# Kernel tuning notes

Hardware: AMD Instinct MI355X
Metric: run time of the kernel (lower is better)

Reference implementation:

```python
import jax, jax.numpy as jnp
import numpy as np

DMODEL = 1024
DK = 64
DHEAD = 16
DEPTH = DK * DHEAD
N, LQ, L = 2, 2048, 2048


def setup_inputs() -> dict:
    key = jax.random.key(0)
    ks = jax.random.split(key, 12)
    s = 1.0 / np.sqrt(DMODEL)
    inp = {
        'x': jax.random.normal(ks[0], (N, LQ, DMODEL), jnp.float32),
        'y': jax.random.normal(ks[1], (N, L, DMODEL), jnp.float32),
        'mask': jnp.tril(jnp.ones((LQ, L), dtype=bool)),  # causal
        'Wq': jax.random.normal(ks[2], (DMODEL, DEPTH), jnp.float32) * s,
        'bq': jnp.zeros((DEPTH,), jnp.float32),
        'Wk': jax.random.normal(ks[3], (DMODEL, DEPTH), jnp.float32) * s,
        'bk': jnp.zeros((DEPTH,), jnp.float32),
        'Wv': jax.random.normal(ks[4], (DMODEL, DEPTH), jnp.float32) * s,
        'bv': jnp.zeros((DEPTH,), jnp.float32),
        'Wo': jax.random.normal(ks[5], (DEPTH, DMODEL), jnp.float32) * (1.0 / np.sqrt(DEPTH)),
        'bo': jnp.zeros((DMODEL,), jnp.float32),
    }
    return inp


def reference(x, y, mask, Wq, bq, Wk, bk, Wv, bv, Wo, bo):
    fac = 1.0 / np.sqrt(DK)
    q = (x @ Wq + bq).reshape(N, LQ, DHEAD, DK).transpose(0, 2, 1, 3)  # N,H,Lq,dk
    k = (y @ Wk + bk).reshape(N, L, DHEAD, DK).transpose(0, 2, 1, 3)   # N,H,L,dk
    v = (y @ Wv + bv).reshape(N, L, DHEAD, DK).transpose(0, 2, 1, 3)   # N,H,L,dk
    scores = jnp.einsum('bhqd,bhkd->bhqk', q, k) * fac                 # N,H,Lq,L
    scores = jnp.where(mask, scores, -1e9)  # mask broadcasts over N,H
    attn = jax.nn.softmax(scores, axis=-1)
    out = jnp.einsum('bhqk,bhkd->bhqd', attn, v)                        # N,H,Lq,dk
    out = out.transpose(0, 2, 1, 3).reshape(N, LQ, DEPTH)
    return out @ Wo + bo
```

## Files before the change

kernel.cpp:

```cpp
#include <hip/hip_runtime.h>
#include <hip/hip_bf16.h>

typedef __attribute__((ext_vector_type(8))) short short8;
typedef __attribute__((ext_vector_type(4))) float floatx4;

#define LQ 2048
#define DM 1024
#define NH 16
#define LOG2E 1.44269504088896f

typedef __attribute__((address_space(1))) void gas_t;
typedef __attribute__((address_space(3))) void las_t;

__device__ __forceinline__ void async16(const __hip_bfloat16* g, __hip_bfloat16* l) {
    __builtin_amdgcn_global_load_lds((gas_t*)g, (las_t*)l, 16, 0, 0);
}

__global__ __launch_bounds__(256) void prep_all(
    const float* __restrict__ x,  const float* __restrict__ y,
    const float* __restrict__ Wq, const float* __restrict__ Wk,
    const float* __restrict__ Wv, const float* __restrict__ Wo,
    __hip_bfloat16* __restrict__ xb,  __hip_bfloat16* __restrict__ yb,
    __hip_bfloat16* __restrict__ Wqt, __hip_bfloat16* __restrict__ Wkt,
    __hip_bfloat16* __restrict__ Wvt, __hip_bfloat16* __restrict__ Wot)
{
    __shared__ float tile[64][65];
    const int t  = threadIdx.x;
    const int bx = blockIdx.x;

    if (bx < 4096) {
        const float* in = (bx < 2048) ? x : y;
        __hip_bfloat16* out = (bx < 2048) ? xb : yb;
        const int i = ((bx & 2047) * 256 + t) * 8;
        float4 a0 = ((const float4*)(in + i))[0];
        float4 a1 = ((const float4*)(in + i))[1];
        union { __hip_bfloat16 h[8]; uint4 u; } pk;
        pk.h[0] = __float2bfloat16(a0.x); pk.h[1] = __float2bfloat16(a0.y);
        pk.h[2] = __float2bfloat16(a0.z); pk.h[3] = __float2bfloat16(a0.w);
        pk.h[4] = __float2bfloat16(a1.x); pk.h[5] = __float2bfloat16(a1.y);
        pk.h[6] = __float2bfloat16(a1.z); pk.h[7] = __float2bfloat16(a1.w);
        *(uint4*)(out + i) = pk.u;
        return;
    }

    const int r    = bx - 4096;
    const int wsel = r >> 8;
    const int tid  = r & 255;
    const int n0   = (tid & 15) * 64, k0 = (tid >> 4) * 64;
    const float* W = (wsel == 0) ? Wq : (wsel == 1) ? Wk : (wsel == 2) ? Wv : Wo;
    __hip_bfloat16* Wt = (wsel == 0) ? Wqt : (wsel == 1) ? Wkt : (wsel == 2) ? Wvt : Wot;

    const int rr0 = t >> 4, c4 = (t & 15) * 4;
#pragma unroll
    for (int rr = 0; rr < 64; rr += 16) {
        float4 v = *(const float4*)&W[(size_t)(k0 + rr0 + rr) * DM + n0 + c4];
        tile[rr0 + rr][c4 + 0] = v.x; tile[rr0 + rr][c4 + 1] = v.y;
        tile[rr0 + rr][c4 + 2] = v.z; tile[rr0 + rr][c4 + 3] = v.w;
    }
    __syncthreads();
    const int nr = t >> 2, kc = (t & 3) * 16;
    union { __hip_bfloat16 h[16]; uint4 u[2]; } pk;
#pragma unroll
    for (int i = 0; i < 16; ++i) pk.h[i] = __float2bfloat16(tile[kc + i][nr]);
    uint4* dst = (uint4*)&Wt[(size_t)(n0 + nr) * DM + k0 + kc];
    dst[0] = pk.u[0];
    dst[1] = pk.u[1];
}

__global__ __launch_bounds__(512, 4) void gemm_qkv(
    const __hip_bfloat16* __restrict__ xb,
    const __hip_bfloat16* __restrict__ yb,
    const __hip_bfloat16* __restrict__ Bt,
    const float* __restrict__ bq, const float* __restrict__ bk,
    const float* __restrict__ bv,
    __hip_bfloat16* __restrict__ Qb, __hip_bfloat16* __restrict__ Kb,
    __hip_bfloat16* __restrict__ Vt,
    float qscl)
{
    constexpr int BM = 256, BN = 128, Kd = 1024;
    constexpr int NHS = Kd / 32;
    __shared__ __align__(16) __hip_bfloat16 As[3][BM * 32];
    __shared__ __align__(16) __hip_bfloat16 Bs[3][BN * 32];

    const int t    = threadIdx.x;
    const int w    = t >> 6;
    const int lane = t & 63;
    const int quad = lane >> 4;
    const int l16  = lane & 15;
    const int wm   = w & 3;
    const int wn   = w >> 2;

    const int f  = blockIdx.x;
    const int rx = f & 7;
    const int rr = f >> 3;
    const int bx = (rx & 3) * 6 + rr % 6;
    const int by = (rx >> 2) * 8 + rr / 6;
    const int m0 = by * BM;
    const int n0 = bx * BN;

    const int region = n0 >> 10;
    const int nl     = n0 & 1023;

    const __hip_bfloat16* A = (region == 0) ? xb : yb;

    floatx4 acc[4][4];
#pragma unroll
    for (int i = 0; i < 4; ++i)
#pragma unroll
        for (int j = 0; j < 4; ++j) acc[i][j] = (floatx4){0.f, 0.f, 0.f, 0.f};

    auto stageA = [&](int h) {
        const int k0 = h * 32, slot = h % 3;
#pragma unroll
        for (int l = 0; l < 2; ++l) {
            const int c   = l * 512 + t;
            const int row = c >> 2;
            const int ch  = (c & 3) ^ ((row >> 1) & 3);
            async16(A + (size_t)(m0 + row) * Kd + k0 + ch * 8, &As[slot][c * 8]);
        }
    };
    auto stageB = [&](int h) {
        const int k0 = h * 32, slot = h % 3;
        const int c   = t;
        const int row = c >> 2;
        const int ch  = (c & 3) ^ ((row >> 1) & 3);
        async16(Bt + (size_t)(n0 + row) * Kd + k0 + ch * 8, &Bs[slot][c * 8]);
    };

    stageA(0); stageB(0); stageA(1); stageB(1);
    asm volatile("s_waitcnt vmcnt(3)" ::: "memory");
    __builtin_amdgcn_sched_barrier(0);
    __builtin_amdgcn_s_barrier();

    const int csw = (l16 >> 1) & 3;

    for (int h = 0; h < NHS; ++h) {
        const int slot = h % 3;
        const __hip_bfloat16* as = &As[slot][0];
        const __hip_bfloat16* bs = &Bs[slot][0];
        short8 af[4], bf[4];

#pragma unroll
        for (int nj = 0; nj < 4; ++nj) {
            const int row = wn * 64 + nj * 16 + l16;
            bf[nj] = *(const short8*)&bs[row * 32 + (quad ^ csw) * 8];
        }
#pragma unroll
        for (int mi = 0; mi < 2; ++mi) {
            const int row = wm * 64 + mi * 16 + l16;
            af[mi] = *(const short8*)&as[row * 32 + (quad ^ csw) * 8];
        }
        if (h + 2 < NHS) stageA(h + 2);
        __builtin_amdgcn_s_barrier();
        asm volatile("s_waitcnt lgkmcnt(0)" ::: "memory");
        __builtin_amdgcn_sched_barrier(0);
        __builtin_amdgcn_s_setprio(1);
#pragma unroll
        for (int mi = 0; mi < 2; ++mi)
#pragma unroll
            for (int nj = 0; nj < 4; ++nj)
                acc[mi][nj] = __builtin_amdgcn_mfma_f32_16x16x32_bf16(af[mi], bf[nj], acc[mi][nj], 0, 0, 0);
        __builtin_amdgcn_s_setprio(0);
        __builtin_amdgcn_s_barrier();

#pragma unroll
        for (int mi = 2; mi < 4; ++mi) {
            const int row = wm * 64 + mi * 16 + l16;
            af[mi] = *(const short8*)&as[row * 32 + (quad ^ csw) * 8];
        }
        if (h + 2 < NHS) stageB(h + 2);
        __builtin_amdgcn_s_barrier();
        asm volatile("s_waitcnt lgkmcnt(0)" ::: "memory");
        __builtin_amdgcn_sched_barrier(0);
        __builtin_amdgcn_s_setprio(1);
#pragma unroll
        for (int mi = 2; mi < 4; ++mi)
#pragma unroll
            for (int nj = 0; nj < 4; ++nj)
                acc[mi][nj] = __builtin_amdgcn_mfma_f32_16x16x32_bf16(af[mi], bf[nj], acc[mi][nj], 0, 0, 0);
        __builtin_amdgcn_s_setprio(0);
        if (h + 2 < NHS)      asm volatile("s_waitcnt vmcnt(3)" ::: "memory");
        else                  asm volatile("s_waitcnt vmcnt(0)" ::: "memory");
        __builtin_amdgcn_sched_barrier(0);
        __builtin_amdgcn_s_barrier();
    }

    if (region < 2) {
        __hip_bfloat16* C    = (region == 0) ? Qb : Kb;
        const float*    bias = (region == 0) ? bq : bk;
        const float     scl  = (region == 0) ? qscl : 1.0f;
#pragma unroll
        for (int j = 0; j < 4; ++j) {
            const int col = nl + wn * 64 + j * 16 + l16;
            const float bvv = bias[col];
#pragma unroll
            for (int mi = 0; mi < 4; ++mi) {
#pragma unroll
                for (int r = 0; r < 4; ++r) {
                    const int row = m0 + wm * 64 + mi * 16 + quad * 4 + r;
                    C[(size_t)row * 1024 + col] = __float2bfloat16((acc[mi][j][r] + bvv) * scl);
                }
            }
        }
    } else {
#pragma unroll
        for (int j = 0; j < 4; ++j) {
            const int col = nl + wn * 64 + j * 16 + l16;
            const float bvv = bv[col];
#pragma unroll
            for (int mi = 0; mi < 4; ++mi) {
                const int row0 = m0 + wm * 64 + mi * 16 + quad * 4;
                union { __hip_bfloat16 h4[4]; uint2 u; } pk;
#pragma unroll
                for (int r = 0; r < 4; ++r)
                    pk.h4[r] = __float2bfloat16(acc[mi][j][r] + bvv);
                *(uint2*)&Vt[((size_t)((row0 >> 11) * 1024 + col)) * 2048 + (row0 & 2047)] = pk.u;
            }
        }
    }
}

__global__ __launch_bounds__(256) void gemm_o(
    const __hip_bfloat16* __restrict__ A,
    const __hip_bfloat16* __restrict__ Bt,
    const float* __restrict__ bias,
    float* __restrict__ C,
    int M)
{
    constexpr int BM = 64, BN = 128, BK = 32, Kd = 1024, NIT = Kd / BK;
    __shared__ __align__(16) __hip_bfloat16 As[3][BM * BK];
    __shared__ __align__(16) __hip_bfloat16 Bs[3][BN * BK];

    const int t    = threadIdx.x;
    const int w    = t >> 6;
    const int lane = t & 63;
    const int quad = lane >> 4;
    const int l16  = lane & 15;
    const int wm   = w & 1;
    const int wn   = w >> 1;

    const int f  = blockIdx.x;
    const int rx = f & 7;
    const int rr = f >> 3;
    const int bx = (rx & 1) * 4 + (rr & 3);
    const int by = (rx >> 1) * 16 + (rr >> 2);
    const int m0 = by * BM;
    const int n0 = bx * BN;

    const int lrow = lane >> 2;
    const int lcol = (lane & 3) * 8;

    floatx4 acc[2][4];
#pragma unroll
    for (int i = 0; i < 2; ++i)
#pragma unroll
        for (int j = 0; j < 4; ++j) acc[i][j] = (floatx4){0.f, 0.f, 0.f, 0.f};

    auto stage = [&](int k0, int buf) {
#pragma unroll
        for (int s = 0; s < 3; ++s) {
            const int seg = w * 3 + s;
            if (seg < 4) {
                async16(A + (size_t)(m0 + seg * 16 + lrow) * Kd + k0 + lcol,
                        &As[buf][seg * 16 * BK]);
            } else {
                const int bs = seg - 4;
                async16(Bt + (size_t)(n0 + bs * 16 + lrow) * Kd + k0 + lcol,
                        &Bs[buf][bs * 16 * BK]);
            }
        }
    };

    stage(0, 0);
    stage(BK, 1);
    int cur = 0;
    for (int i = 0; i < NIT; ++i) {
        if (i < NIT - 1) asm volatile("s_waitcnt vmcnt(3)" ::: "memory");
        else             asm volatile("s_waitcnt vmcnt(0)" ::: "memory");
        __builtin_amdgcn_sched_barrier(0);
        __builtin_amdgcn_s_barrier();
        if (i + 2 < NIT) stage((i + 2) * BK, (cur + 2 >= 3) ? cur - 1 : cur + 2);

        short8 af[2], bf[4];
#pragma unroll
        for (int ii = 0; ii < 2; ++ii)
            af[ii] = *(const short8*)&As[cur][(wm * 32 + ii * 16 + l16) * BK + quad * 8];
#pragma unroll
        for (int j = 0; j < 4; ++j)
            bf[j] = *(const short8*)&Bs[cur][(wn * 64 + j * 16 + l16) * BK + quad * 8];
#pragma unroll
        for (int ii = 0; ii < 2; ++ii)
#pragma unroll
            for (int j = 0; j < 4; ++j)
                acc[ii][j] = __builtin_amdgcn_mfma_f32_16x16x32_bf16(af[ii], bf[j], acc[ii][j], 0, 0, 0);
        cur = (cur + 1 >= 3) ? 0 : cur + 1;
    }

#pragma unroll
    for (int j = 0; j < 4; ++j) {
        const int col = n0 + wn * 64 + j * 16 + l16;
        const float bvf = bias[col];
#pragma unroll
        for (int i = 0; i < 2; ++i) {
#pragma unroll
            for (int r = 0; r < 4; ++r) {
                const int row = m0 + wm * 32 + i * 16 + quad * 4 + r;
                C[(size_t)row * 1024 + col] = acc[i][j][r] + bvf;
            }
        }
    }
}

template <bool A_IS_F32, bool OUT_F32, bool TRANSV = false>
__global__ __launch_bounds__(256) void gemm64(
    const void* __restrict__ Av,
    const float* __restrict__ B,
    const float* __restrict__ bias,
    void* __restrict__ Cv,
    int M, int N, int K, float scale)
{
    __shared__ __align__(16) __hip_bfloat16 As[64][40];
    __shared__ __align__(16) __hip_bfloat16 Bs[64][40];

    const int t    = threadIdx.x;
    const int wave = t >> 6;
    const int lane = t & 63;
    const int quad = lane >> 4;
    const int l16  = lane & 15;
    const int m0   = blockIdx.y * 64;
    const int n0   = blockIdx.x * 64;

    floatx4 acc[4];
#pragma unroll
    for (int i = 0; i < 4; ++i) acc[i] = (floatx4){0.f, 0.f, 0.f, 0.f};

    const int arow = t >> 2, acol = (t & 3) * 8;
    const int bkk  = t >> 3, bnn  = (t & 7) * 8;

    for (int k0 = 0; k0 < K; k0 += 32) {
        if constexpr (A_IS_F32) {
            const float* A = (const float*)Av;
            const float* ap = A + (size_t)(m0 + arow) * K + k0 + acol;
            float4 a0 = ((const float4*)ap)[0];
            float4 a1 = ((const float4*)ap)[1];
            union { __hip_bfloat16 h[8]; short8 s; } up;
            up.h[0] = __float2bfloat16(a0.x); up.h[1] = __float2bfloat16(a0.y);
            up.h[2] = __float2bfloat16(a0.z); up.h[3] = __float2bfloat16(a0.w);
            up.h[4] = __float2bfloat16(a1.x); up.h[5] = __float2bfloat16(a1.y);
            up.h[6] = __float2bfloat16(a1.z); up.h[7] = __float2bfloat16(a1.w);
            *(short8*)(&As[arow][acol]) = up.s;
        } else {
            const __hip_bfloat16* A = (const __hip_bfloat16*)Av;
            uint4 av = *(const uint4*)(A + (size_t)(m0 + arow) * K + k0 + acol);
            *(uint4*)(&As[arow][acol]) = av;
        }
        {
            const float* bp = B + (size_t)(k0 + bkk) * N + n0 + bnn;
            float4 b0 = ((const float4*)bp)[0];
            float4 b1 = ((const float4*)bp)[1];
            Bs[bnn + 0][bkk] = __float2bfloat16(b0.x);
            Bs[bnn + 1][bkk] = __float2bfloat16(b0.y);
            Bs[bnn + 2][bkk] = __float2bfloat16(b0.z);
            Bs[bnn + 3][bkk] = __float2bfloat16(b0.w);
            Bs[bnn + 4][bkk] = __float2bfloat16(b1.x);
            Bs[bnn + 5][bkk] = __float2bfloat16(b1.y);
            Bs[bnn + 6][bkk] = __float2bfloat16(b1.z);
            Bs[bnn + 7][bkk] = __float2bfloat16(b1.w);
        }
        __syncthreads();

        short8 afrag = *(const short8*)(&As[wave * 16 + l16][quad * 8]);
#pragma unroll
        for (int nt = 0; nt < 4; ++nt) {
            short8 bfrag = *(const short8*)(&Bs[nt * 16 + l16][quad * 8]);
            acc[nt] = __builtin_amdgcn_mfma_f32_16x16x32_bf16(afrag, bfrag, acc[nt], 0, 0, 0);
        }
        __syncthreads();
    }

#pragma unroll
    for (int nt = 0; nt < 4; ++nt) {
        const int col = n0 + nt * 16 + l16;
        const float bvf = bias[col];
        if constexpr (TRANSV) {
            const int row0 = m0 + wave * 16 + quad * 4;
            union { __hip_bfloat16 h4[4]; uint2 u; } pk;
#pragma unroll
            for (int r = 0; r < 4; ++r)
                pk.h4[r] = __float2bfloat16(acc[nt][r] + bvf);
            *(uint2*)&((__hip_bfloat16*)Cv)[((size_t)((row0 >> 11) * 1024 + col)) * 2048 + (row0 & 2047)] = pk.u;
        } else {
#pragma unroll
            for (int r = 0; r < 4; ++r) {
                const int row = m0 + wave * 16 + quad * 4 + r;
                const float v = (acc[nt][r] + bvf) * scale;
                if constexpr (OUT_F32) ((float*)Cv)[(size_t)row * N + col] = v;
                else ((__hip_bfloat16*)Cv)[(size_t)row * N + col] = __float2bfloat16(v);
            }
        }
    }
}

#define PP 72

__global__ __launch_bounds__(256, 2) void attn_mfma11(
    const __hip_bfloat16* __restrict__ Q,
    const __hip_bfloat16* __restrict__ K,
    const __hip_bfloat16* __restrict__ Vt,
    __hip_bfloat16* __restrict__ O)
{
    __shared__ __align__(16) __hip_bfloat16 KtS[3][64 * 64];
    __shared__ __align__(16) __hip_bfloat16 VtS[4][64 * 64];
    __shared__ __align__(16) __hip_bfloat16 PsQ[128 * PP];

    const int t    = threadIdx.x;
    const int w    = t >> 6;
    const int lane = t & 63;
    const int quad = lane >> 4;
    const int l16  = lane & 15;

    const int f   = blockIdx.x;
    const int xcd = f & 7;
    const int u   = f >> 3;
    const int pi  = u >> 4;
    const int qr  = u & 15;
    const int qx  = (pi & 2) ? (15 - qr) : qr;
    const int p   = xcd * 4 + pi;
    const int h   = p & 15;
    const int b   = p >> 4;
    const int q0  = qx * 128;

    const size_t rowbase = (size_t)b * LQ;
    const int    hcol    = h * 64;
    const size_t vbase   = (size_t)(b * NH + h) * 64 * LQ;

    const int r8 = l16 & 7;

    auto stage = [&](int j0n, int jtile) {
        const int ks = jtile % 3;
        const int vs = jtile & 3;
#pragma unroll
        for (int rnd = 0; rnd < 2; ++rnd) {
            const int c   = rnd * 256 + t;
            const int row = c >> 3;
            const int ch  = (c & 7) ^ (row & 7);
            async16(K + (rowbase + j0n + row) * DM + hcol + ch * 8,
                    &KtS[ks][c * 8]);
            async16(Vt + vbase + (size_t)row * LQ + j0n + ch * 8,
                    &VtS[vs][c * 8]);
        }
    };

    {
        const int qrow = t >> 1, qseg = (t & 1) * 32;
        const uint4* src = (const uint4*)(Q + (rowbase + q0 + qrow) * DM + hcol + qseg);
        uint4* dst = (uint4*)&PsQ[qrow * PP + qseg];
        dst[0] = src[0]; dst[1] = src[1]; dst[2] = src[2]; dst[3] = src[3];
    }
    stage(0, 0);
    stage(64, 1);

    short8 qf[2][2];
#pragma unroll
    for (int g = 0; g < 2; ++g)
#pragma unroll
        for (int hh = 0; hh < 2; ++hh)
            qf[g][hh] = *(const short8*)&PsQ[(w * 32 + g * 16 + l16) * PP + hh * 32 + quad * 8];

    __hip_bfloat16* Pw = &PsQ[(w * 32) * PP];

    float l_i[2] = {0.f, 0.f};
    floatx4 o[2][4];
#pragma unroll
    for (int g = 0; g < 2; ++g)
#pragma unroll
        for (int i = 0; i < 4; ++i) o[g][i] = (floatx4){0.f, 0.f, 0.f, 0.f};

    const int wq_lo  = q0 + w * 32;
    const int wq_hi  = wq_lo + 31;
    const int ntiles = 2 * qx + 2;

    short8 pa[2][2];
    int    pslot = -1;

    for (int jt = 0; jt < ntiles; ++jt) {
        const int j0 = jt * 64;

        if (jt < ntiles - 1) asm volatile("s_waitcnt vmcnt(4)" ::: "memory");
        else                 asm volatile("s_waitcnt vmcnt(0)" ::: "memory");
        __builtin_amdgcn_sched_barrier(0);
        __builtin_amdgcn_s_barrier();
        if (jt + 2 < ntiles) stage(j0 + 128, jt + 2);

        const bool active = (j0 <= wq_hi);

        short8 ak[4][2];
        if (active) {
#pragma unroll
            for (int jc = 0; jc < 4; ++jc) {
                const __hip_bfloat16* kr = &KtS[jt % 3][(jc * 16 + l16) * 64];
                ak[jc][0] = *(const short8*)&kr[((quad    ) ^ r8) * 8];
                ak[jc][1] = *(const short8*)&kr[((quad + 4) ^ r8) * 8];
            }
        }

        if (pslot >= 0) {
            __builtin_amdgcn_s_setprio(1);
#pragma unroll
            for (int subf = 0; subf < 4; ++subf) {
                const __hip_bfloat16* vr = &VtS[pslot][(subf * 16 + l16) * 64];
                short8 vb0 = *(const short8*)&vr[((quad    ) ^ r8) * 8];
                short8 vb1 = *(const short8*)&vr[((quad + 4) ^ r8) * 8];
#pragma unroll
                for (int g = 0; g < 2; ++g) {
                    o[g][subf] = __builtin_amdgcn_mfma_f32_16x16x32_bf16(pa[g][0], vb0, o[g][subf], 0, 0, 0);
                    o[g][subf] = __builtin_amdgcn_mfma_f32_16x16x32_bf16(pa[g][1], vb1, o[g][subf], 0, 0, 0);
                }
            }
            __builtin_amdgcn_s_setprio(0);
            pslot = -1;
        }

        if (active) {
            const bool bnd = (j0 + 63 > wq_lo);
            __builtin_amdgcn_s_setprio(1);
#pragma unroll
            for (int jc = 0; jc < 4; ++jc) {
#pragma unroll
                for (int g = 0; g < 2; ++g) {
                    floatx4 z = (floatx4){0.f, 0.f, 0.f, 0.f};
                    z = __builtin_amdgcn_mfma_f32_16x16x32_bf16(ak[jc][0], qf[g][0], z, 0, 0, 0);
                    z = __builtin_amdgcn_mfma_f32_16x16x32_bf16(ak[jc][1], qf[g][1], z, 0, 0, 0);
                    if (bnd) {
                        const int qg = wq_lo + g * 16 + l16;
#pragma unroll
                        for (int r = 0; r < 4; ++r) {
                            const int j = j0 + jc * 16 + quad * 4 + r;
                            if (j > qg) z[r] = -1e30f;
                        }
                    }
                    union { __hip_bfloat16 h4[4]; uint2 u; } pk;
#pragma unroll
                    for (int r = 0; r < 4; ++r) {
                        const float e = __builtin_amdgcn_exp2f(z[r]);
                        l_i[g] += e;
                        pk.h4[r] = __float2bfloat16(e);
                    }
                    *(uint2*)&Pw[(g * 16 + l16) * PP + jc * 16 + quad * 4] = pk.u;
                }
            }
            __builtin_amdgcn_s_setprio(0);
#pragma unroll
            for (int g = 0; g < 2; ++g) {
                pa[g][0] = *(const short8*)&Pw[(g * 16 + l16) * PP + quad * 8];
                pa[g][1] = *(const short8*)&Pw[(g * 16 + l16) * PP + 32 + quad * 8];
            }
            pslot = jt & 3;
        }
    }

    if (pslot >= 0) {
#pragma unroll
        for (int subf = 0; subf < 4; ++subf) {
            const __hip_bfloat16* vr = &VtS[pslot][(subf * 16 + l16) * 64];
            short8 vb0 = *(const short8*)&vr[((quad    ) ^ r8) * 8];
            short8 vb1 = *(const short8*)&vr[((quad + 4) ^ r8) * 8];
#pragma unroll
            for (int g = 0; g < 2; ++g) {
                o[g][subf] = __builtin_amdgcn_mfma_f32_16x16x32_bf16(pa[g][0], vb0, o[g][subf], 0, 0, 0);
                o[g][subf] = __builtin_amdgcn_mfma_f32_16x16x32_bf16(pa[g][1], vb1, o[g][subf], 0, 0, 0);
            }
        }
    }

#pragma unroll
    for (int g = 0; g < 2; ++g) {
        l_i[g] += __shfl_xor(l_i[g], 16);
        l_i[g] += __shfl_xor(l_i[g], 32);
#pragma unroll
        for (int r = 0; r < 4; ++r) {
            const float linv = 1.0f / __shfl(l_i[g], quad * 4 + r);
            const size_t row = rowbase + q0 + w * 32 + g * 16 + quad * 4 + r;
#pragma unroll
            for (int subf = 0; subf < 4; ++subf)
                O[row * DM + hcol + subf * 16 + l16] = __float2bfloat16(o[g][subf][r] * linv);
        }
    }
}

extern "C" void kernel_launch(void* const* d_in, const int* in_sizes, int n_in,
                              void* d_out, int out_size, void* d_ws, size_t ws_size,
                              hipStream_t stream)
{
    (void)in_sizes; (void)n_in; (void)out_size;

    const float* x  = (const float*)d_in[0];
    const float* y  = (const float*)d_in[1];
    const float* Wq = (const float*)d_in[3];
    const float* bq = (const float*)d_in[4];
    const float* Wk = (const float*)d_in[5];
    const float* bk = (const float*)d_in[6];
    const float* Wv = (const float*)d_in[7];
    const float* bv = (const float*)d_in[8];
    const float* Wo = (const float*)d_in[9];
    const float* bo = (const float*)d_in[10];

    const size_t NTOK = (size_t)2 * LQ * DM;
    const size_t MM   = (size_t)DM * DM;
    const int    M    = 2 * LQ;
    const float  QSCL = 0.125f * LOG2E;

    __hip_bfloat16* Qb  = (__hip_bfloat16*)d_ws;
    __hip_bfloat16* Kb  = Qb + NTOK;
    __hip_bfloat16* Vtb = Kb + NTOK;
    __hip_bfloat16* Ab  = Vtb + NTOK;

    const size_t need = (4 * NTOK + 2 * NTOK + 4 * MM) * sizeof(__hip_bfloat16);
    const dim3 agrid(512, 1, 1);

    if (ws_size >= need) {
        __hip_bfloat16* xb  = Ab + NTOK;
        __hip_bfloat16* yb  = xb + NTOK;
        __hip_bfloat16* Wqt = yb + NTOK;
        __hip_bfloat16* Wkt = Wqt + MM;
        __hip_bfloat16* Wvt = Wkt + MM;
        __hip_bfloat16* Wot = Wvt + MM;
        (void)Wkt; (void)Wvt;

        prep_all<<<5120, 256, 0, stream>>>(x, y, Wq, Wk, Wv, Wo,
                                           xb, yb, Wqt, Wkt, Wvt, Wot);

        gemm_qkv<<<384, 512, 0, stream>>>(xb, yb, Wqt, bq, bk, bv, Qb, Kb, Vtb, QSCL);
        attn_mfma11<<<agrid, 256, 0, stream>>>(Qb, Kb, Vtb, Ab);
        gemm_o<<<512, 256, 0, stream>>>(Ab, Wot, bo, (float*)d_out, M);
    } else {
        const dim3 gblk(DM / 64, M / 64);
        gemm64<true,  false><<<gblk, 256, 0, stream>>>(x, Wq, bq, Qb, M, DM, DM, QSCL);
        gemm64<true,  false><<<gblk, 256, 0, stream>>>(y, Wk, bk, Kb, M, DM, DM, 1.0f);
        gemm64<true,  false, true><<<gblk, 256, 0, stream>>>(y, Wv, bv, Vtb, M, DM, DM, 1.0f);
        attn_mfma11<<<agrid, 256, 0, stream>>>(Qb, Kb, Vtb, Ab);
        gemm64<false, true ><<<gblk, 256, 0, stream>>>(Ab, Wo, bo, (float*)d_out, M, DM, DM, 1.0f);
    }
}
```

Baseline: 208.9 us.

## Split attention block across 8 waves of 16 query rows each

The attention kernel now runs 512 threads per block, with each wave owning 16 query rows instead of 32. Staging loads are spread over twice as many threads, and per-wave registers for Q fragments, accumulators and P are halved. The aim is more waves in flight to hide latency and finer causal skipping per wave. In exchange, each wave gets less MFMA reuse of K/V fragments read from LDS, doubling LDS reads per FLOP, and it raises barrier participation cost.

```diff
diff --git a/kernel.cpp b/kernel.cpp
--- a/kernel.cpp
+++ b/kernel.cpp
@@ -403,7 +403,7 @@
 
 #define PP 72
 
-__global__ __launch_bounds__(256, 2) void attn_mfma11(
+__global__ __launch_bounds__(512, 4) void attn_mfma12(
     const __hip_bfloat16* __restrict__ Q,
     const __hip_bfloat16* __restrict__ K,
     const __hip_bfloat16* __restrict__ Vt,
@@ -439,54 +439,47 @@
     auto stage = [&](int j0n, int jtile) {
         const int ks = jtile % 3;
         const int vs = jtile & 3;
-#pragma unroll
-        for (int rnd = 0; rnd < 2; ++rnd) {
-            const int c   = rnd * 256 + t;
-            const int row = c >> 3;
-            const int ch  = (c & 7) ^ (row & 7);
-            async16(K + (rowbase + j0n + row) * DM + hcol + ch * 8,
-                    &KtS[ks][c * 8]);
-            async16(Vt + vbase + (size_t)row * LQ + j0n + ch * 8,
-                    &VtS[vs][c * 8]);
-        }
+        const int c   = t;
+        const int row = c >> 3;
+        const int ch  = (c & 7) ^ (row & 7);
+        async16(K + (rowbase + j0n + row) * DM + hcol + ch * 8,
+                &KtS[ks][c * 8]);
+        async16(Vt + vbase + (size_t)row * LQ + j0n + ch * 8,
+                &VtS[vs][c * 8]);
     };
 
     {
-        const int qrow = t >> 1, qseg = (t & 1) * 32;
+        const int qrow = t >> 2, qseg = (t & 3) * 16;
         const uint4* src = (const uint4*)(Q + (rowbase + q0 + qrow) * DM + hcol + qseg);
         uint4* dst = (uint4*)&PsQ[qrow * PP + qseg];
-        dst[0] = src[0]; dst[1] = src[1]; dst[2] = src[2]; dst[3] = src[3];
+        dst[0] = src[0]; dst[1] = src[1];
     }
     stage(0, 0);
     stage(64, 1);
 
-    short8 qf[2][2];
-#pragma unroll
-    for (int g = 0; g < 2; ++g)
-#pragma unroll
-        for (int hh = 0; hh < 2; ++hh)
-            qf[g][hh] = *(const short8*)&PsQ[(w * 32 + g * 16 + l16) * PP + hh * 32 + quad * 8];
-
-    __hip_bfloat16* Pw = &PsQ[(w * 32) * PP];
-
-    float l_i[2] = {0.f, 0.f};
-    floatx4 o[2][4];
-#pragma unroll
-    for (int g = 0; g < 2; ++g)
-#pragma unroll
-        for (int i = 0; i < 4; ++i) o[g][i] = (floatx4){0.f, 0.f, 0.f, 0.f};
-
-    const int wq_lo  = q0 + w * 32;
-    const int wq_hi  = wq_lo + 31;
+    short8 qf[2];
+#pragma unroll
+    for (int hh = 0; hh < 2; ++hh)
+        qf[hh] = *(const short8*)&PsQ[(w * 16 + l16) * PP + hh * 32 + quad * 8];
+
+    __hip_bfloat16* Pw = &PsQ[(w * 16) * PP];
+
+    float l_i = 0.f;
+    floatx4 o[4];
+#pragma unroll
+    for (int i = 0; i < 4; ++i) o[i] = (floatx4){0.f, 0.f, 0.f, 0.f};
+
+    const int wq_lo  = q0 + w * 16;
+    const int wq_hi  = wq_lo + 15;
     const int ntiles = 2 * qx + 2;
 
-    short8 pa[2][2];
+    short8 pa[2];
     int    pslot = -1;
 
     for (int jt = 0; jt < ntiles; ++jt) {
         const int j0 = jt * 64;
 
-        if (jt < ntiles - 1) asm volatile("s_waitcnt vmcnt(4)" ::: "memory");
+        if (jt < ntiles - 1) asm volatile("s_waitcnt vmcnt(2)" ::: "memory");
         else                 asm volatile("s_waitcnt vmcnt(0)" ::: "memory");
         __builtin_amdgcn_sched_barrier(0);
         __builtin_amdgcn_s_barrier();
@@ -511,11 +504,8 @@
                 const __hip_bfloat16* vr = &VtS[pslot][(subf * 16 + l16) * 64];
                 short8 vb0 = *(const short8*)&vr[((quad    ) ^ r8) * 8];
                 short8 vb1 = *(const short8*)&vr[((quad + 4) ^ r8) * 8];
-#pragma unroll
-                for (int g = 0; g < 2; ++g) {
-                    o[g][subf] = __builtin_amdgcn_mfma_f32_16x16x32_bf16(pa[g][0], vb0, o[g][subf], 0, 0, 0);
-                    o[g][subf] = __builtin_amdgcn_mfma_f32_16x16x32_bf16(pa[g][1], vb1, o[g][subf], 0, 0, 0);
-                }
+                o[subf] = __builtin_amdgcn_mfma_f32_16x16x32_bf16(pa[0], vb0, o[subf], 0, 0, 0);
+                o[subf] = __builtin_amdgcn_mfma_f32_16x16x32_bf16(pa[1], vb1, o[subf], 0, 0, 0);
             }
             __builtin_amdgcn_s_setprio(0);
             pslot = -1;
@@ -526,35 +516,29 @@
             __builtin_amdgcn_s_setprio(1);
 #pragma unroll
             for (int jc = 0; jc < 4; ++jc) {
-#pragma unroll
-                for (int g = 0; g < 2; ++g) {
-                    floatx4 z = (floatx4){0.f, 0.f, 0.f, 0.f};
-                    z = __builtin_amdgcn_mfma_f32_16x16x32_bf16(ak[jc][0], qf[g][0], z, 0, 0, 0);
-                    z = __builtin_amdgcn_mfma_f32_16x16x32_bf16(ak[jc][1], qf[g][1], z, 0, 0, 0);
-                    if (bnd) {
-                        const int qg = wq_lo + g * 16 + l16;
-#pragma unroll
-                        for (int r = 0; r < 4; ++r) {
-                            const int j = j0 + jc * 16 + quad * 4 + r;
-                            if (j > qg) z[r] = -1e30f;
-                        }
+                floatx4 z = (floatx4){0.f, 0.f, 0.f, 0.f};
+                z = __builtin_amdgcn_mfma_f32_16x16x32_bf16(ak[jc][0], qf[0], z, 0, 0, 0);
+                z = __builtin_amdgcn_mfma_f32_16x16x32_bf16(ak[jc][1], qf[1], z, 0, 0, 0);
+                if (bnd) {
+                    const int qg = wq_lo + l16;
+#pragma unroll
+                    for (int r = 0; r < 4; ++r) {
+                        const int j = j0 + jc * 16 + quad * 4 + r;
+                        if (j > qg) z[r] = -1e30f;
                     }
-                    union { __hip_bfloat16 h4[4]; uint2 u; } pk;
-#pragma unroll
-                    for (int r = 0; r < 4; ++r) {
-                        const float e = __builtin_amdgcn_exp2f(z[r]);
-                        l_i[g] += e;
-                        pk.h4[r] = __float2bfloat16(e);
-                    }
-                    *(uint2*)&Pw[(g * 16 + l16) * PP + jc * 16 + quad * 4] = pk.u;
                 }
+                union { __hip_bfloat16 h4[4]; uint2 u; } pk;
+#pragma unroll
+                for (int r = 0; r < 4; ++r) {
+                    const float e = __builtin_amdgcn_exp2f(z[r]);
+                    l_i += e;
+                    pk.h4[r] = __float2bfloat16(e);
+                }
+                *(uint2*)&Pw[l16 * PP + jc * 16 + quad * 4] = pk.u;
             }
             __builtin_amdgcn_s_setprio(0);
-#pragma unroll
-            for (int g = 0; g < 2; ++g) {
-                pa[g][0] = *(const short8*)&Pw[(g * 16 + l16) * PP + quad * 8];
-                pa[g][1] = *(const short8*)&Pw[(g * 16 + l16) * PP + 32 + quad * 8];
-            }
+            pa[0] = *(const short8*)&Pw[l16 * PP + quad * 8];
+            pa[1] = *(const short8*)&Pw[l16 * PP + 32 + quad * 8];
             pslot = jt & 3;
         }
     }
@@ -565,26 +549,20 @@
             const __hip_bfloat16* vr = &VtS[pslot][(subf * 16 + l16) * 64];
             short8 vb0 = *(const short8*)&vr[((quad    ) ^ r8) * 8];
             short8 vb1 = *(const short8*)&vr[((quad + 4) ^ r8) * 8];
-#pragma unroll
-            for (int g = 0; g < 2; ++g) {
-                o[g][subf] = __builtin_amdgcn_mfma_f32_16x16x32_bf16(pa[g][0], vb0, o[g][subf], 0, 0, 0);
-                o[g][subf] = __builtin_amdgcn_mfma_f32_16x16x32_bf16(pa[g][1], vb1, o[g][subf], 0, 0, 0);
-            }
-        }
-    }
-
-#pragma unroll
-    for (int g = 0; g < 2; ++g) {
-        l_i[g] += __shfl_xor(l_i[g], 16);
-        l_i[g] += __shfl_xor(l_i[g], 32);
-#pragma unroll
-        for (int r = 0; r < 4; ++r) {
-            const float linv = 1.0f / __shfl(l_i[g], quad * 4 + r);
-            const size_t row = rowbase + q0 + w * 32 + g * 16 + quad * 4 + r;
-#pragma unroll
-            for (int subf = 0; subf < 4; ++subf)
-                O[row * DM + hcol + subf * 16 + l16] = __float2bfloat16(o[g][subf][r] * linv);
-        }
+            o[subf] = __builtin_amdgcn_mfma_f32_16x16x32_bf16(pa[0], vb0, o[subf], 0, 0, 0);
+            o[subf] = __builtin_amdgcn_mfma_f32_16x16x32_bf16(pa[1], vb1, o[subf], 0, 0, 0);
+        }
+    }
+
+    l_i += __shfl_xor(l_i, 16);
+    l_i += __shfl_xor(l_i, 32);
+#pragma unroll
+    for (int r = 0; r < 4; ++r) {
+        const float linv = 1.0f / __shfl(l_i, quad * 4 + r);
+        const size_t row = rowbase + q0 + w * 16 + quad * 4 + r;
+#pragma unroll
+        for (int subf = 0; subf < 4; ++subf)
+            O[row * DM + hcol + subf * 16 + l16] = __float2bfloat16(o[subf][r] * linv);
     }
 }
 
@@ -631,14 +609,14 @@
                                            xb, yb, Wqt, Wkt, Wvt, Wot);
 
         gemm_qkv<<<384, 512, 0, stream>>>(xb, yb, Wqt, bq, bk, bv, Qb, Kb, Vtb, QSCL);
-        attn_mfma11<<<agrid, 256, 0, stream>>>(Qb, Kb, Vtb, Ab);
+        attn_mfma12<<<agrid, 512, 0, stream>>>(Qb, Kb, Vtb, Ab);
         gemm_o<<<512, 256, 0, stream>>>(Ab, Wot, bo, (float*)d_out, M);
     } else {
         const dim3 gblk(DM / 64, M / 64);
         gemm64<true,  false><<<gblk, 256, 0, stream>>>(x, Wq, bq, Qb, M, DM, DM, QSCL);
         gemm64<true,  false><<<gblk, 256, 0, stream>>>(y, Wk, bk, Kb, M, DM, DM, 1.0f);
         gemm64<true,  false, true><<<gblk, 256, 0, stream>>>(y, Wv, bv, Vtb, M, DM, DM, 1.0f);
-        attn_mfma11<<<agrid, 256, 0, stream>>>(Qb, Kb, Vtb, Ab);
+        attn_mfma12<<<agrid, 512, 0, stream>>>(Qb, Kb, Vtb, Ab);
         gemm64<false, true ><<<gblk, 256, 0, stream>>>(Ab, Wo, bo, (float*)d_out, M, DM, DM, 1.0f);
     }
 }
```

Result: faster. 201.7 us (-3.4%).
